# Optimization experiments

Measured on AMD Instinct MI355X. Metric: run time of the kernel, lower is better.

Reference implementation:

```python
import jax, jax.numpy as jnp
import numpy as np

D_MODEL = 1024
N_HEADS = 16
D_K = D_MODEL // N_HEADS
MAX_REL = 128
SCALE = 1.0 / np.sqrt(D_K)
TEMP = 1.0


def setup_inputs() -> dict:
    key = jax.random.key(0)
    ks = jax.random.split(key, 12)
    B, S = 4, 1024
    inp = {
        "query": jax.random.normal(ks[0], (B, S, D_MODEL), jnp.float32),
        "key": jax.random.normal(ks[1], (B, S, D_MODEL), jnp.float32),
        "value": jax.random.normal(ks[2], (B, S, D_MODEL), jnp.float32),
        "mask": jnp.ones((B, S), jnp.int32),
        "w_q": jax.random.normal(ks[3], (D_MODEL, D_MODEL), jnp.float32) * 0.03,
        "b_q": jnp.zeros((D_MODEL,), jnp.float32),
        "w_k": jax.random.normal(ks[4], (D_MODEL, D_MODEL), jnp.float32) * 0.03,
        "b_k": jnp.zeros((D_MODEL,), jnp.float32),
        "w_v": jax.random.normal(ks[5], (D_MODEL, D_MODEL), jnp.float32) * 0.03,
        "b_v": jnp.zeros((D_MODEL,), jnp.float32),
        "w_o": jax.random.normal(ks[6], (D_MODEL, D_MODEL), jnp.float32) * 0.03,
        "b_o": jnp.zeros((D_MODEL,), jnp.float32),
        "rel_k": jax.random.normal(ks[7], (2 * MAX_REL + 1, D_K), jnp.float32),
        "rel_v": jax.random.normal(ks[8], (2 * MAX_REL + 1, D_K), jnp.float32),
    }
    return inp


def _relative_positions(seq_len):
    pos = jnp.arange(seq_len)
    rel = pos[None, :] - pos[:, None]  # [S, S]
    return jnp.clip(rel, -MAX_REL, MAX_REL) + MAX_REL


def reference(query, key, value, mask, w_q, b_q, w_k, b_k, w_v, b_v, w_o, b_o, rel_k, rel_v):
    B, S, _ = query.shape
    # projections (torch Linear: x @ W.T + b)
    Q = (query @ w_q.T + b_q).reshape(B, S, N_HEADS, D_K).transpose(0, 2, 1, 3)  # [B,H,S,d]
    K = (key @ w_k.T + b_k).reshape(B, S, N_HEADS, D_K).transpose(0, 2, 1, 3)
    V = (value @ w_v.T + b_v).reshape(B, S, N_HEADS, D_K).transpose(0, 2, 1, 3)

    scores = jnp.einsum("bhld,bhrd->bhlr", Q, K) * SCALE  # [B,H,S,S]

    rel_idx = _relative_positions(S)                      # [S,S] int
    rpk = rel_k[rel_idx]                                  # [S,S,d]
    scores = scores + jnp.einsum("bhld,lrd->bhlr", Q, rpk)

    scores = scores / TEMP
    m = mask[:, None, None, :]                            # [B,1,1,S]
    scores = jnp.where(m == 0, -1e9, scores)

    attn = jax.nn.softmax(scores, axis=-1)                # [B,H,S,S]
    context = jnp.einsum("bhlr,bhrd->bhld", attn, V)
    rpv = rel_v[rel_idx]                                  # [S,S,d]
    context = context + jnp.einsum("bhlr,lrd->bhld", attn, rpv)

    context = context.transpose(0, 2, 1, 3).reshape(B, S, D_MODEL)
    out = context @ w_o.T + b_o
    return out
```

## Files before the change

kernel.cpp:

```cpp
#include <hip/hip_runtime.h>
#include <hip/hip_bf16.h>

#define S_LEN  1024
#define DMODEL 1024
#define NHEADS 16
#define DK     64
#define SCALE  0.125f

typedef __bf16 bf16x8_t __attribute__((ext_vector_type(8)));
typedef __bf16 bf16x4_t __attribute__((ext_vector_type(4)));
typedef float  f32x4_t  __attribute__((ext_vector_type(4)));

#define MFMA16(A, B, C) __builtin_amdgcn_mfma_f32_16x16x32_bf16((A), (B), (C), 0, 0, 0)

__device__ __forceinline__ void async16(const void* g, void* l) {
    __builtin_amdgcn_global_load_lds(
        (const __attribute__((address_space(1))) unsigned int*)g,
        (__attribute__((address_space(3))) unsigned int*)l, 16, 0, 0);
}

__global__ __launch_bounds__(256) void cast_all_kernel(
    const float* __restrict__ q, const float* __restrict__ k, const float* __restrict__ v,
    const float* __restrict__ wq, const float* __restrict__ wk,
    const float* __restrict__ wv, const float* __restrict__ wo,
    const float* __restrict__ relk, const float* __restrict__ relv,
    __bf16* __restrict__ Xbf, __bf16* __restrict__ Wall,
    __bf16* __restrict__ relkp, __bf16* __restrict__ rvT,
    __bf16* __restrict__ Wqlo)
{
    const long i = (long)blockIdx.x * 256 + threadIdx.x;
    if (i < 3145728) {
        const int z   = (int)(i >> 20);
        const long rem = i & 1048575;
        const float4 s = ((const float4*)(z == 0 ? q : (z == 1 ? k : v)))[rem];
        bf16x4_t h;
        h[0] = (__bf16)s.x; h[1] = (__bf16)s.y; h[2] = (__bf16)s.z; h[3] = (__bf16)s.w;
        *(bf16x4_t*)(Xbf + ((size_t)z << 22) + rem * 4) = h;
    } else if (i < 3145728 + 1048576) {
        const long wi = i - 3145728;
        const int z   = (int)(wi >> 18);
        const long rem = wi & 262143;
        const float* src = (z == 0) ? wq : (z == 1) ? wk : (z == 2) ? wv : wo;
        const float4 s = ((const float4*)src)[rem];
        const float xs[4] = {s.x, s.y, s.z, s.w};
        bf16x4_t h;
        #pragma unroll
        for (int t = 0; t < 4; ++t) h[t] = (__bf16)xs[t];
        *(bf16x4_t*)(Wall + ((size_t)z << 20) + rem * 4) = h;
        if (z == 0) {
            bf16x4_t l;
            #pragma unroll
            for (int t = 0; t < 4; ++t) l[t] = (__bf16)(xs[t] - (float)h[t]);
            *(bf16x4_t*)(Wqlo + rem * 4) = l;
        }
    } else if (i < 3145728 + 1048576 + 4352) {
        const long ri = i - (3145728 + 1048576);
        const int j  = (int)(ri >> 4);
        const int d4 = (int)(ri & 15) * 4;
        bf16x4_t h, l;
        if (j < 257) {
            const float4 s = *(const float4*)(relk + j * 64 + d4);
            const float xs[4] = {s.x, s.y, s.z, s.w};
            #pragma unroll
            for (int t = 0; t < 4; ++t) {
                h[t] = (__bf16)xs[t];
                l[t] = (__bf16)(xs[t] - (float)h[t]);
            }
        } else {
            #pragma unroll
            for (int t = 0; t < 4; ++t) { h[t] = (__bf16)0.f; l[t] = (__bf16)0.f; }
        }
        *(bf16x4_t*)(relkp + j * 64 + d4) = h;
        *(bf16x4_t*)(relkp + 17408 + j * 64 + d4) = l;
    } else if (i < 3145728 + 1048576 + 4352 + 4608) {
        const long ri = i - (3145728 + 1048576 + 4352);
        const int d  = (int)(ri / 72);
        const int j4 = (int)(ri % 72) * 4;
        bf16x4_t o;
        #pragma unroll
        for (int t = 0; t < 4; ++t) {
            const int j = j4 + t;
            o[t] = (j < 257) ? (__bf16)relv[j * 64 + d] : (__bf16)0.f;
        }
        *(bf16x4_t*)(rvT + d * 288 + j4) = o;
    }
}

__device__ __forceinline__ void gemm128_core(
    const __bf16* __restrict__ A, const __bf16* __restrict__ W,
    __bf16* As, __bf16* Ws, f32x4_t acc[4][4])
{
    const int tid  = threadIdx.x;
    const int lane = tid & 63;
    const int quad = lane >> 4;
    const int l15  = lane & 15;
    const int wid  = tid >> 6;
    const int wm = wid >> 1, wn = wid & 1;

    for (int kt = 0; kt < 32; ++kt) {
        #pragma unroll
        for (int r = 0; r < 2; ++r) {
            const int c = r * 256 + tid;
            const int row = c >> 2, kb = c & 3;
            async16(A + row * 1024 + kt * 32 + kb * 8, As + c * 8);
            async16(W + row * 1024 + kt * 32 + kb * 8, Ws + c * 8);
        }
        __syncthreads();
        bf16x8_t af[4], wf[4];
        #pragma unroll
        for (int i = 0; i < 4; ++i) {
            af[i] = *(const bf16x8_t*)(As + (wm * 64 + i * 16 + l15) * 32 + quad * 8);
            wf[i] = *(const bf16x8_t*)(Ws + (wn * 64 + i * 16 + l15) * 32 + quad * 8);
        }
        #pragma unroll
        for (int i = 0; i < 4; ++i)
            #pragma unroll
            for (int j = 0; j < 4; ++j)
                acc[i][j] = MFMA16(af[i], wf[j], acc[i][j]);
        __syncthreads();
    }
}

__global__ __launch_bounds__(256) void gemm_qkv_kernel(
    const __bf16* __restrict__ Xbf, const __bf16* __restrict__ Wall,
    const __bf16* __restrict__ Wqlo,
    const float* __restrict__ bq, const float* __restrict__ bk, const float* __restrict__ bv,
    __bf16* __restrict__ QKVh)
{
    __shared__ __bf16 As[4096], Ws[4096];
    const int z = blockIdx.z;
    const __bf16* A = Xbf + (size_t)z * 4194304 + (size_t)blockIdx.y * 131072;
    const __bf16* W = Wall + (size_t)z * 1048576 + (size_t)blockIdx.x * 131072;
    f32x4_t acc[4][4];
    #pragma unroll
    for (int i = 0; i < 4; ++i)
        #pragma unroll
        for (int j = 0; j < 4; ++j)
            acc[i][j] = (f32x4_t){0.f, 0.f, 0.f, 0.f};

    gemm128_core(A, W, As, Ws, acc);
    if (z == 0)
        gemm128_core(A, Wqlo + (size_t)blockIdx.x * 131072, As, Ws, acc);

    const int tid = threadIdx.x, lane = tid & 63, quad = lane >> 4, l15 = lane & 15;
    const int wid = tid >> 6, wm = wid >> 1, wn = wid & 1;
    const int m0 = blockIdx.y * 128 + wm * 64;
    const int n0 = blockIdx.x * 128 + wn * 64;
    const float* bias = (z == 0) ? bq : ((z == 1) ? bk : bv);
    __bf16* dst = QKVh + (size_t)z * 4194304;

    if (z < 2) {
        #pragma unroll
        for (int j = 0; j < 4; ++j) {
            const int n = n0 + j * 16 + l15;
            const float bn = bias[n];
            #pragma unroll
            for (int i = 0; i < 4; ++i) {
                #pragma unroll
                for (int v = 0; v < 4; ++v) {
                    const int m = m0 + i * 16 + quad * 4 + v;
                    dst[((((m >> 10) * 16 + (n >> 6)) << 16)) + ((m & 1023) << 6) + (n & 63)]
                        = (__bf16)(acc[i][j][v] + bn);
                }
            }
        }
    } else {
        #pragma unroll
        for (int j = 0; j < 4; ++j) {
            const int n = n0 + j * 16 + l15;
            const float bn = bias[n];
            #pragma unroll
            for (int i = 0; i < 4; ++i) {
                const int m = m0 + i * 16 + quad * 4;
                bf16x4_t pk;
                #pragma unroll
                for (int v = 0; v < 4; ++v) pk[v] = (__bf16)(acc[i][j][v] + bn);
                const int s = m & 1023, d = n & 63;
                const size_t idx = (((size_t)((m >> 10) * 16 + (n >> 6))) << 16)
                                 + (size_t)(s >> 5) * 2048 + d * 32 + (s & 31);
                *(bf16x4_t*)(dst + idx) = pk;
            }
        }
    }
}

__global__ __launch_bounds__(256) void gemm_out_kernel(
    const __bf16* __restrict__ ctx, const __bf16* __restrict__ Wo,
    const float* __restrict__ bo, float* __restrict__ out)
{
    __shared__ __bf16 As[4096], Ws[4096];
    const __bf16* A = ctx + (size_t)blockIdx.y * 131072;
    const __bf16* W = Wo + (size_t)blockIdx.x * 131072;
    f32x4_t acc[4][4];
    #pragma unroll
    for (int i = 0; i < 4; ++i)
        #pragma unroll
        for (int j = 0; j < 4; ++j)
            acc[i][j] = (f32x4_t){0.f, 0.f, 0.f, 0.f};
    gemm128_core(A, W, As, Ws, acc);

    const int tid = threadIdx.x, lane = tid & 63, quad = lane >> 4, l15 = lane & 15;
    const int wid = tid >> 6, wm = wid >> 1, wn = wid & 1;
    const int m0 = blockIdx.y * 128 + wm * 64;
    const int n0 = blockIdx.x * 128 + wn * 64;
    #pragma unroll
    for (int j = 0; j < 4; ++j) {
        const int n = n0 + j * 16 + l15;
        const float bn = bo[n];
        #pragma unroll
        for (int i = 0; i < 4; ++i)
            #pragma unroll
            for (int v = 0; v < 4; ++v) {
                const int m = m0 + i * 16 + quad * 4 + v;
                out[(size_t)m * 1024 + n] = acc[i][j][v] + bn;
            }
    }
}

__global__ __launch_bounds__(256, 2) void attn_fused_kernel(
    const __bf16* __restrict__ Qh, const __bf16* __restrict__ Kh,
    const __bf16* __restrict__ Vt, const __bf16* __restrict__ relkp,
    const __bf16* __restrict__ rvT, const int* __restrict__ mask,
    const float* __restrict__ relv, __bf16* __restrict__ ctx)
{
    __shared__ __align__(16) __bf16 Ks[3][2048];
    __shared__ __align__(16) __bf16 Vs[3][2048];
    __shared__ __align__(16) __bf16 p_s[4][16][40];
    __shared__ __align__(16) __bf16 w_s[4][16][256];
    __shared__ __align__(16) __bf16 madd_sb[1024];

    const int tid = threadIdx.x, lane = tid & 63, wid = tid >> 6;
    const int quad = lane >> 4, l15 = lane & 15;
    const int lin = blockIdx.x;
    const int slot = lin >> 3;
    const int bh = (lin & 7) + 8 * (slot >> 4);
    const int chunk = slot & 15;
    const int b = bh >> 4;
    const int t0w = chunk * 4 + wid;
    const int l0 = t0w * 16;

    const __bf16* Qbase = Qh + (size_t)bh * 65536;
    const __bf16* Kbase = Kh + (size_t)bh * 65536;
    const __bf16* Vbase = Vt + (size_t)bh * 65536;
    const int* maskb = mask + b * 1024;
    const __bf16* rlo = relkp + 17408;

    int gKo[2], lKo[2], gVo[2], lVo[2];
    #pragma unroll
    for (int ii = 0; ii < 2; ++ii) {
        const int chK = (wid & 1) * 128 + ii * 64 + lane;
        const int rK = chK >> 3, pK = chK & 7, gK = pK ^ (rK & 7);
        gKo[ii] = rK * 64 + gK * 8;
        lKo[ii] = chK * 8;
        const int chV = (wid & 1) * 128 + ii * 64 + lane;
        const int dV = chV >> 2, pV = chV & 3, gV = pV ^ ((dV >> 1) & 3);
        gVo[ii] = dV * 32 + gV * 8;
        lVo[ii] = chV * 8;
    }

    #define STAGE(t, buf)                                                     \
        do {                                                                  \
            if (wid < 2) {                                                    \
                async16(Kbase + (t) * 2048 + gKo[0], &Ks[buf][0] + lKo[0]);   \
                async16(Kbase + (t) * 2048 + gKo[1], &Ks[buf][0] + lKo[1]);   \
            } else {                                                          \
                async16(Vbase + (t) * 2048 + gVo[0], &Vs[buf][0] + lVo[0]);   \
                async16(Vbase + (t) * 2048 + gVo[1], &Vs[buf][0] + lVo[1]);   \
            }                                                                 \
        } while (0)

    STAGE(0, 0);
    STAGE(1, 1);

    {
        const int4 mv = *(const int4*)(maskb + tid * 4);
        madd_sb[tid * 4 + 0] = mv.x ? (__bf16)0.f : (__bf16)-1.0e9f;
        madd_sb[tid * 4 + 1] = mv.y ? (__bf16)0.f : (__bf16)-1.0e9f;
        madd_sb[tid * 4 + 2] = mv.z ? (__bf16)0.f : (__bf16)-1.0e9f;
        madd_sb[tid * 4 + 3] = mv.w ? (__bf16)0.f : (__bf16)-1.0e9f;
    }

    const bf16x8_t aq0 = *(const bf16x8_t*)(Qbase + (l0 + l15) * 64 + quad * 8);
    const bf16x8_t aq1 = *(const bf16x8_t*)(Qbase + (l0 + l15) * 64 + 32 + quad * 8);

    float c0[4], c1[4];
    {
        const int jr = (l15 == 1) ? 256 : 0;
        const bf16x8_t bh0 = *(const bf16x8_t*)(relkp + jr * 64 + quad * 8);
        const bf16x8_t bh1 = *(const bf16x8_t*)(relkp + jr * 64 + 32 + quad * 8);
        const bf16x8_t bl0 = *(const bf16x8_t*)(rlo + jr * 64 + quad * 8);
        const bf16x8_t bl1 = *(const bf16x8_t*)(rlo + jr * 64 + 32 + quad * 8);
        f32x4_t cr = (f32x4_t){0.f, 0.f, 0.f, 0.f};
        cr = MFMA16(aq0, bl0, cr);
        cr = MFMA16(aq1, bl1, cr);
        cr = MFMA16(aq0, bh0, cr);
        cr = MFMA16(aq1, bh1, cr);
        #pragma unroll
        for (int v = 0; v < 4; ++v) {
            c0[v] = __shfl(cr[v], (lane & 48), 64);
            c1[v] = __shfl(cr[v], (lane & 48) | 1, 64);
        }
    }

    {
        uint4* wz = (uint4*)&w_s[wid][0][0];
        for (int t = lane; t < 512; t += 64) wz[t] = (uint4){0u, 0u, 0u, 0u};
    }

    f32x4_t o[4];
    #pragma unroll
    for (int dt = 0; dt < 4; ++dt) o[dt] = (f32x4_t){0.f, 0.f, 0.f, 0.f};
    float rowsum[4] = {0.f, 0.f, 0.f, 0.f};
    float e0[4] = {0.f, 0.f, 0.f, 0.f};
    float e1[4] = {0.f, 0.f, 0.f, 0.f};
    f32x4_t qb_carry = (f32x4_t){0.f, 0.f, 0.f, 0.f};

    __syncthreads();

    for (int pc = 0; pc < 32; ++pc) {
        if (pc < 31) asm volatile("s_waitcnt vmcnt(2)" ::: "memory");
        else         asm volatile("s_waitcnt vmcnt(0)" ::: "memory");
        asm volatile("" ::: "memory");
        __builtin_amdgcn_s_barrier();
        asm volatile("" ::: "memory");
        if (pc + 2 < 32) STAGE(pc + 2, (pc + 2) % 3);

        __builtin_amdgcn_s_setprio(1);
        const int cur = pc % 3;
        const int rb0 = pc * 32;
        const int tI0 = pc * 2;
        #pragma unroll
        for (int sl = 0; sl < 2; ++sl) {
            const int tI = tI0 + sl;
            const int dist = tI - t0w;
            const int R = sl * 16 + l15;
            const bf16x8_t kb0 =
                *(const bf16x8_t*)(&Ks[cur][0] + R * 64 + (quad ^ (R & 7)) * 8);
            const bf16x8_t kb1 =
                *(const bf16x8_t*)(&Ks[cur][0] + R * 64 + (((quad + 4) ^ (R & 7))) * 8);
            f32x4_t s = (f32x4_t){0.f, 0.f, 0.f, 0.f};
            s = MFMA16(aq0, kb0, s);
            s = MFMA16(aq1, kb1, s);
            const float madd = (float)madd_sb[rb0 + R];

            if (dist <= -9 || dist >= 9) {
                const bool isLo = dist < 0;
                #pragma unroll
                for (int v = 0; v < 4; ++v) {
                    const float cc = isLo ? c0[v] : c1[v];
                    const float p = __expf(fmaf(s[v], SCALE, cc) + madd);
                    const __bf16 pb = (__bf16)p;
                    const float pf = (float)pb;
                    rowsum[v] += pf;
                    if (isLo) e0[v] += pf; else e1[v] += pf;
                    p_s[wid][quad * 4 + v][sl * 16 + l15] = pb;
                }
            } else {
                const int base = dist * 16 + 128;
                f32x4_t qbA;
                const bool seed = (dist == -8) || (tI == 0);
                if (seed) {
                    int ra = base - 15 + l15;
                    ra = ra < 0 ? 0 : (ra > 256 ? 256 : ra);
                    const bf16x8_t hA0 = *(const bf16x8_t*)(relkp + ra * 64 + quad * 8);
                    const bf16x8_t hA1 = *(const bf16x8_t*)(relkp + ra * 64 + 32 + quad * 8);
                    const bf16x8_t lA0 = *(const bf16x8_t*)(rlo + ra * 64 + quad * 8);
                    const bf16x8_t lA1 = *(const bf16x8_t*)(rlo + ra * 64 + 32 + quad * 8);
                    qbA = (f32x4_t){0.f, 0.f, 0.f, 0.f};
                    qbA = MFMA16(aq0, lA0, qbA);
                    qbA = MFMA16(aq1, lA1, qbA);
                    qbA = MFMA16(aq0, hA0, qbA);
                    qbA = MFMA16(aq1, hA1, qbA);
                } else {
                    qbA = qb_carry;
                }
                int rb2 = base + 1 + l15;
                rb2 = rb2 > 256 ? 256 : rb2;
                const bf16x8_t hB0 = *(const bf16x8_t*)(relkp + rb2 * 64 + quad * 8);
                const bf16x8_t hB1 = *(const bf16x8_t*)(relkp + rb2 * 64 + 32 + quad * 8);
                const bf16x8_t lB0 = *(const bf16x8_t*)(rlo + rb2 * 64 + quad * 8);
                const bf16x8_t lB1 = *(const bf16x8_t*)(rlo + rb2 * 64 + 32 + quad * 8);
                f32x4_t qbB = (f32x4_t){0.f, 0.f, 0.f, 0.f};
                qbB = MFMA16(aq0, lB0, qbB);
                qbB = MFMA16(aq1, lB1, qbB);
                qbB = MFMA16(aq0, hB0, qbB);
                qbB = MFMA16(aq1, hB1, qbB);
                qb_carry = qbB;
                #pragma unroll
                for (int v = 0; v < 4; ++v) {
                    const int lrow = quad * 4 + v;
                    const int c = l15 + 15 - lrow;
                    const int src = (lane & 48) | (c & 15);
                    const float bA = __shfl(qbA[v], src, 64);
                    const float bB = __shfl(qbB[v], src, 64);
                    const float qbv = (c & 16) ? bB : bA;
                    const int j = base + l15 - lrow;
                    const float bias = (j < 0) ? c0[v] : ((j > 256) ? c1[v] : qbv);
                    const float p = __expf(fmaf(s[v], SCALE, bias) + madd);
                    const __bf16 pb = (__bf16)p;
                    const float pf = (float)pb;
                    rowsum[v] += pf;
                    p_s[wid][lrow][sl * 16 + l15] = pb;
                    if (j <= 0)        e0[v] += pf;
                    else if (j >= 256) e1[v] += pf;
                    else               w_s[wid][lrow][j] = pb;
                }
            }
        }
        const bf16x8_t pa = *(const bf16x8_t*)(&p_s[wid][l15][quad * 8]);
        #pragma unroll
        for (int dt = 0; dt < 4; ++dt) {
            const int D = dt * 16 + l15;
            const bf16x8_t vb =
                *(const bf16x8_t*)(&Vs[cur][0] + D * 32 + ((quad ^ ((D >> 1) & 3))) * 8);
            o[dt] = MFMA16(pa, vb, o[dt]);
        }
        __builtin_amdgcn_s_setprio(0);
    }
    #undef STAGE

    for (int kc = 0; kc < 8; ++kc) {
        const bf16x8_t wa = *(const bf16x8_t*)(&w_s[wid][l15][kc * 32 + quad * 8]);
        #pragma unroll
        for (int dt = 0; dt < 4; ++dt) {
            const bf16x8_t rb =
                *(const bf16x8_t*)(rvT + (dt * 16 + l15) * 288 + kc * 32 + quad * 8);
            o[dt] = MFMA16(wa, rb, o[dt]);
        }
    }

    #pragma unroll
    for (int v = 0; v < 4; ++v) {
        #pragma unroll
        for (int mm = 1; mm < 16; mm <<= 1) {
            rowsum[v] += __shfl_xor(rowsum[v], mm, 64);
            e0[v]     += __shfl_xor(e0[v], mm, 64);
            e1[v]     += __shfl_xor(e1[v], mm, 64);
        }
    }

    float rinv[4];
    #pragma unroll
    for (int v = 0; v < 4; ++v)
        rinv[v] = 1.f / rowsum[v];
    const int h = bh & 15;
    #pragma unroll
    for (int dt = 0; dt < 4; ++dt) {
        const int d = dt * 16 + l15;
        const float rv0   = relv[d];
        const float rv256 = relv[256 * 64 + d];
        #pragma unroll
        for (int v = 0; v < 4; ++v) {
            const int lrow = quad * 4 + v;
            const float val = (o[dt][v] + e0[v] * rv0 + e1[v] * rv256) * rinv[v];
            ctx[((size_t)b * 1024 + l0 + lrow) * 1024 + h * 64 + d] = (__bf16)val;
        }
    }
}

extern "C" void kernel_launch(void* const* d_in, const int* in_sizes, int n_in,
                              void* d_out, int out_size, void* d_ws, size_t ws_size,
                              hipStream_t stream)
{
    const float* q    = (const float*)d_in[0];
    const float* k    = (const float*)d_in[1];
    const float* v    = (const float*)d_in[2];
    const int*   mask = (const int*)  d_in[3];
    const float* wq   = (const float*)d_in[4];
    const float* bq   = (const float*)d_in[5];
    const float* wk   = (const float*)d_in[6];
    const float* bk   = (const float*)d_in[7];
    const float* wv   = (const float*)d_in[8];
    const float* bv   = (const float*)d_in[9];
    const float* wo   = (const float*)d_in[10];
    const float* bo   = (const float*)d_in[11];
    const float* relk = (const float*)d_in[12];
    const float* relv = (const float*)d_in[13];

    __bf16* Xbf   = (__bf16*)d_ws;
    __bf16* Xgap  = Xbf   + 12582912;
    __bf16* Wqlo  = Xgap  + 4194304;
    __bf16* Wall  = Wqlo  + 1048576;
    __bf16* QKVh  = Wall  + 4194304;
    __bf16* ctx   = QKVh  + 12582912;
    __bf16* relkp = ctx   + 4194304;
    __bf16* rvT   = relkp + 34816;

    cast_all_kernel<<<16419, 256, 0, stream>>>(q, k, v, wq, wk, wv, wo, relk, relv,
                                               Xbf, Wall, relkp, rvT, Wqlo);
    gemm_qkv_kernel<<<dim3(8, 32, 3), 256, 0, stream>>>(Xbf, Wall, Wqlo,
                                                        bq, bk, bv, QKVh);
    attn_fused_kernel<<<1024, 256, 0, stream>>>(QKVh, QKVh + 4194304,
                                                QKVh + 2 * 4194304, relkp,
                                                rvT, mask, relv, ctx);
    gemm_out_kernel<<<dim3(8, 32, 1), 256, 0, stream>>>(ctx, Wall + 3 * 1048576,
                                                        bo, (float*)d_out);
}
```

Before: 302.5 us.

## Prefetch relative-key band loads early and fuse Q hi/lo GEMM passes

```diff
diff --git a/kernel.cpp b/kernel.cpp
--- a/kernel.cpp
+++ b/kernel.cpp
@@ -121,13 +121,53 @@
     }
 }
 
+__device__ __forceinline__ void gemm128_core_dual(
+    const __bf16* __restrict__ A, const __bf16* __restrict__ W,
+    const __bf16* __restrict__ W2,
+    __bf16* As, __bf16* Ws, __bf16* Ws2, f32x4_t acc[4][4])
+{
+    const int tid  = threadIdx.x;
+    const int lane = tid & 63;
+    const int quad = lane >> 4;
+    const int l15  = lane & 15;
+    const int wid  = tid >> 6;
+    const int wm = wid >> 1, wn = wid & 1;
+
+    for (int kt = 0; kt < 32; ++kt) {
+        #pragma unroll
+        for (int r = 0; r < 2; ++r) {
+            const int c = r * 256 + tid;
+            const int row = c >> 2, kb = c & 3;
+            async16(A  + row * 1024 + kt * 32 + kb * 8, As  + c * 8);
+            async16(W  + row * 1024 + kt * 32 + kb * 8, Ws  + c * 8);
+            async16(W2 + row * 1024 + kt * 32 + kb * 8, Ws2 + c * 8);
+        }
+        __syncthreads();
+        bf16x8_t af[4], wf[4], wg[4];
+        #pragma unroll
+        for (int i = 0; i < 4; ++i) {
+            af[i] = *(const bf16x8_t*)(As  + (wm * 64 + i * 16 + l15) * 32 + quad * 8);
+            wf[i] = *(const bf16x8_t*)(Ws  + (wn * 64 + i * 16 + l15) * 32 + quad * 8);
+            wg[i] = *(const bf16x8_t*)(Ws2 + (wn * 64 + i * 16 + l15) * 32 + quad * 8);
+        }
+        #pragma unroll
+        for (int i = 0; i < 4; ++i)
+            #pragma unroll
+            for (int j = 0; j < 4; ++j) {
+                acc[i][j] = MFMA16(af[i], wg[j], acc[i][j]);
+                acc[i][j] = MFMA16(af[i], wf[j], acc[i][j]);
+            }
+        __syncthreads();
+    }
+}
+
 __global__ __launch_bounds__(256) void gemm_qkv_kernel(
     const __bf16* __restrict__ Xbf, const __bf16* __restrict__ Wall,
     const __bf16* __restrict__ Wqlo,
     const float* __restrict__ bq, const float* __restrict__ bk, const float* __restrict__ bv,
     __bf16* __restrict__ QKVh)
 {
-    __shared__ __bf16 As[4096], Ws[4096];
+    __shared__ __bf16 As[4096], Ws[4096], Ws2[4096];
     const int z = blockIdx.z;
     const __bf16* A = Xbf + (size_t)z * 4194304 + (size_t)blockIdx.y * 131072;
     const __bf16* W = Wall + (size_t)z * 1048576 + (size_t)blockIdx.x * 131072;
@@ -138,9 +178,11 @@
         for (int j = 0; j < 4; ++j)
             acc[i][j] = (f32x4_t){0.f, 0.f, 0.f, 0.f};
 
-    gemm128_core(A, W, As, Ws, acc);
     if (z == 0)
-        gemm128_core(A, Wqlo + (size_t)blockIdx.x * 131072, As, Ws, acc);
+        gemm128_core_dual(A, W, Wqlo + (size_t)blockIdx.x * 131072,
+                          As, Ws, Ws2, acc);
+    else
+        gemm128_core(A, W, As, Ws, acc);
 
     const int tid = threadIdx.x, lane = tid & 63, quad = lane >> 4, l15 = lane & 15;
     const int wid = tid >> 6, wm = wid >> 1, wn = wid & 1;
@@ -226,7 +268,7 @@
     __shared__ __align__(16) __bf16 Ks[3][2048];
     __shared__ __align__(16) __bf16 Vs[3][2048];
     __shared__ __align__(16) __bf16 p_s[4][16][40];
-    __shared__ __align__(16) __bf16 w_s[4][16][256];
+    __shared__ __align__(16) __bf16 w_s[4][16][260];
     __shared__ __align__(16) __bf16 madd_sb[1024];
 
     const int tid = threadIdx.x, lane = tid & 63, wid = tid >> 6;
@@ -304,7 +346,7 @@
 
     {
         uint4* wz = (uint4*)&w_s[wid][0][0];
-        for (int t = lane; t < 512; t += 64) wz[t] = (uint4){0u, 0u, 0u, 0u};
+        for (int t = lane; t < 520; t += 64) wz[t] = (uint4){0u, 0u, 0u, 0u};
     }
 
     f32x4_t o[4];
@@ -323,16 +365,56 @@
         asm volatile("" ::: "memory");
         __builtin_amdgcn_s_barrier();
         asm volatile("" ::: "memory");
+
+        const int tIa = pc * 2, tIb = tIa + 1;
+        const int da = tIa - t0w, db = tIb - t0w;
+        const bool bandA = (da >= -8) && (da <= 8);
+        const bool bandB = (db >= -8) && (db <= 8);
+        bf16x8_t sA_h0, sA_h1, sA_l0, sA_l1;
+        bf16x8_t b0_h0, b0_h1, b0_l0, b0_l1;
+        bf16x8_t b1_h0, b1_h1, b1_l0, b1_l1;
+        if (bandA) {
+            int rb2 = da * 16 + 129 + l15;
+            rb2 = rb2 > 256 ? 256 : rb2;
+            b0_h0 = *(const bf16x8_t*)(relkp + rb2 * 64 + quad * 8);
+            b0_h1 = *(const bf16x8_t*)(relkp + rb2 * 64 + 32 + quad * 8);
+            b0_l0 = *(const bf16x8_t*)(rlo + rb2 * 64 + quad * 8);
+            b0_l1 = *(const bf16x8_t*)(rlo + rb2 * 64 + 32 + quad * 8);
+            if (da == -8 || tIa == 0) {
+                int ra = da * 16 + 113 + l15;
+                ra = ra < 0 ? 0 : (ra > 256 ? 256 : ra);
+                sA_h0 = *(const bf16x8_t*)(relkp + ra * 64 + quad * 8);
+                sA_h1 = *(const bf16x8_t*)(relkp + ra * 64 + 32 + quad * 8);
+                sA_l0 = *(const bf16x8_t*)(rlo + ra * 64 + quad * 8);
+                sA_l1 = *(const bf16x8_t*)(rlo + ra * 64 + 32 + quad * 8);
+            }
+        }
+        if (bandB) {
+            int rb2 = db * 16 + 129 + l15;
+            rb2 = rb2 > 256 ? 256 : rb2;
+            b1_h0 = *(const bf16x8_t*)(relkp + rb2 * 64 + quad * 8);
+            b1_h1 = *(const bf16x8_t*)(relkp + rb2 * 64 + 32 + quad * 8);
+            b1_l0 = *(const bf16x8_t*)(rlo + rb2 * 64 + quad * 8);
+            b1_l1 = *(const bf16x8_t*)(rlo + rb2 * 64 + 32 + quad * 8);
+            if (db == -8) {
+                int ra = db * 16 + 113 + l15;
+                ra = ra < 0 ? 0 : (ra > 256 ? 256 : ra);
+                sA_h0 = *(const bf16x8_t*)(relkp + ra * 64 + quad * 8);
+                sA_h1 = *(const bf16x8_t*)(relkp + ra * 64 + 32 + quad * 8);
+                sA_l0 = *(const bf16x8_t*)(rlo + ra * 64 + quad * 8);
+                sA_l1 = *(const bf16x8_t*)(rlo + ra * 64 + 32 + quad * 8);
+            }
+        }
+
         if (pc + 2 < 32) STAGE(pc + 2, (pc + 2) % 3);
 
         __builtin_amdgcn_s_setprio(1);
         const int cur = pc % 3;
         const int rb0 = pc * 32;
-        const int tI0 = pc * 2;
         #pragma unroll
         for (int sl = 0; sl < 2; ++sl) {
-            const int tI = tI0 + sl;
-            const int dist = tI - t0w;
+            const int tI = (sl == 0) ? tIa : tIb;
+            const int dist = (sl == 0) ? da : db;
             const int R = sl * 16 + l15;
             const bf16x8_t kb0 =
                 *(const bf16x8_t*)(&Ks[cur][0] + R * 64 + (quad ^ (R & 7)) * 8);
@@ -360,31 +442,19 @@
                 f32x4_t qbA;
                 const bool seed = (dist == -8) || (tI == 0);
                 if (seed) {
-                    int ra = base - 15 + l15;
-                    ra = ra < 0 ? 0 : (ra > 256 ? 256 : ra);
-                    const bf16x8_t hA0 = *(const bf16x8_t*)(relkp + ra * 64 + quad * 8);
-                    const bf16x8_t hA1 = *(const bf16x8_t*)(relkp + ra * 64 + 32 + quad * 8);
-                    const bf16x8_t lA0 = *(const bf16x8_t*)(rlo + ra * 64 + quad * 8);
-                    const bf16x8_t lA1 = *(const bf16x8_t*)(rlo + ra * 64 + 32 + quad * 8);
                     qbA = (f32x4_t){0.f, 0.f, 0.f, 0.f};
-                    qbA = MFMA16(aq0, lA0, qbA);
-                    qbA = MFMA16(aq1, lA1, qbA);
-                    qbA = MFMA16(aq0, hA0, qbA);
-                    qbA = MFMA16(aq1, hA1, qbA);
+                    qbA = MFMA16(aq0, sA_l0, qbA);
+                    qbA = MFMA16(aq1, sA_l1, qbA);
+                    qbA = MFMA16(aq0, sA_h0, qbA);
+                    qbA = MFMA16(aq1, sA_h1, qbA);
                 } else {
                     qbA = qb_carry;
                 }
-                int rb2 = base + 1 + l15;
-                rb2 = rb2 > 256 ? 256 : rb2;
-                const bf16x8_t hB0 = *(const bf16x8_t*)(relkp + rb2 * 64 + quad * 8);
-                const bf16x8_t hB1 = *(const bf16x8_t*)(relkp + rb2 * 64 + 32 + quad * 8);
-                const bf16x8_t lB0 = *(const bf16x8_t*)(rlo + rb2 * 64 + quad * 8);
-                const bf16x8_t lB1 = *(const bf16x8_t*)(rlo + rb2 * 64 + 32 + quad * 8);
                 f32x4_t qbB = (f32x4_t){0.f, 0.f, 0.f, 0.f};
-                qbB = MFMA16(aq0, lB0, qbB);
-                qbB = MFMA16(aq1, lB1, qbB);
-                qbB = MFMA16(aq0, hB0, qbB);
-                qbB = MFMA16(aq1, hB1, qbB);
+                qbB = MFMA16(aq0, sl ? b1_l0 : b0_l0, qbB);
+                qbB = MFMA16(aq1, sl ? b1_l1 : b0_l1, qbB);
+                qbB = MFMA16(aq0, sl ? b1_h0 : b0_h0, qbB);
+                qbB = MFMA16(aq1, sl ? b1_h1 : b0_h1, qbB);
                 qb_carry = qbB;
                 #pragma unroll
                 for (int v = 0; v < 4; ++v) {
```

Result: no change. 307.7 us (+1.7%).
